# Performance work log

Measured on AMD Instinct MI355X. Metric: run time of the kernel, lower is better.

## Reference

```python
import math
import jax, jax.numpy as jnp
import numpy as np

N_HEADS = 16
TOPK_FACTOR = 0.5

def setup_inputs() -> dict:
    key = jax.random.key(0)
    ks = jax.random.split(key, 11)
    B, L, D = 2, 2048, 1024
    s = 0.02
    return {
        "q": jax.random.normal(ks[0], (B, L, D), jnp.float32),
        "k": jax.random.normal(ks[1], (B, L, D), jnp.float32),
        "v": jax.random.normal(ks[2], (B, L, D), jnp.float32),
        "Wq": jax.random.normal(ks[3], (D, D), jnp.float32) * s,
        "bq": jnp.zeros((D,), jnp.float32),
        "Wk": jax.random.normal(ks[4], (D, D), jnp.float32) * s,
        "bk": jnp.zeros((D,), jnp.float32),
        "Wv": jax.random.normal(ks[5], (D, D), jnp.float32) * s,
        "bv": jnp.zeros((D,), jnp.float32),
        "Wo": jax.random.normal(ks[6], (D, D), jnp.float32) * s,
        "bo": jnp.zeros((D,), jnp.float32),
    }

def reference(q, k, v, Wq, bq, Wk, bk, Wv, bv, Wo, bo):
    B, Lq, D = q.shape
    Lk = k.shape[1]
    H = N_HEADS
    d_k = D // H
    # projections -> [B, H, L, d_k]
    Q = (q @ Wq.T + bq).reshape(B, Lq, H, d_k).transpose(0, 2, 1, 3)
    K = (k @ Wk.T + bk).reshape(B, Lk, H, d_k).transpose(0, 2, 1, 3)
    V = (v @ Wv.T + bv).reshape(B, Lk, H, d_k).transpose(0, 2, 1, 3)
    # dense scores [B, H, Lq, Lk]
    scores = jnp.einsum("bhqd,bhkd->bhqk", Q, K) / math.sqrt(d_k)
    topk = max(1, int(TOPK_FACTOR * Lk))
    topk_scores, topk_idx = jax.lax.top_k(scores, topk)  # [B,H,Lq,topk]
    sm = jax.nn.softmax(topk_scores, axis=-1)
    # scatter softmax probs back into a zero [B,H,Lq,Lk] tensor (dropout in eval = identity)
    b_idx = jnp.arange(B)[:, None, None, None]
    h_idx = jnp.arange(H)[None, :, None, None]
    q_idx = jnp.arange(Lq)[None, None, :, None]
    attn = jnp.zeros_like(scores).at[b_idx, h_idx, q_idx, topk_idx].set(sm)
    ctx = jnp.einsum("bhqk,bhkd->bhqd", attn, V)
    ctx = ctx.transpose(0, 2, 1, 3).reshape(B, Lq, H * d_k)
    return ctx @ Wo.T + bo
```

## Files before the change

### kernel.cpp

```cpp
#include <hip/hip_runtime.h>
#include <math.h>

#define BATCH 2
#define SEQ 2048
#define DM 1024
#define NH 16
#define DH 64
#define TOPKN 1024
#define MROWS (BATCH * SEQ)

typedef float f32x4 __attribute__((ext_vector_type(4)));
typedef short s16x8 __attribute__((ext_vector_type(8)));
typedef short s16x4 __attribute__((ext_vector_type(4)));

#if __has_builtin(__builtin_amdgcn_mfma_f32_16x16x16_bf16)
#define MFMA1616(acc, a, b) acc = __builtin_amdgcn_mfma_f32_16x16x16_bf16(a, b, acc, 0, 0, 0)
#define MFMA1616_FENCE()
#elif __has_builtin(__builtin_amdgcn_mfma_f32_16x16x16bf16_1k)
#define MFMA1616(acc, a, b) acc = __builtin_amdgcn_mfma_f32_16x16x16bf16_1k(a, b, acc, 0, 0, 0)
#define MFMA1616_FENCE()
#else
#define MFMA1616(acc, a, b) \
  asm volatile("v_mfma_f32_16x16x16_bf16 %0, %1, %2, %0" : "+v"(acc) : "v"(a), "v"(b))
#define MFMA1616_FENCE() asm volatile("s_nop 7\ns_nop 7")
#endif

__device__ __forceinline__ unsigned short f2bf(float x) {
  unsigned u = __float_as_uint(x);
  return (unsigned short)((u + 0x7FFFu + ((u >> 16) & 1u)) >> 16);
}
__device__ __forceinline__ unsigned packHL(float x) {
  unsigned h = f2bf(x);
  float r = x - __uint_as_float(h << 16);
  unsigned l = f2bf(r);
  return h | (l << 16);
}

__global__ __launch_bounds__(256) void convW(const float* __restrict__ W,
                                             unsigned short* __restrict__ Whi,
                                             unsigned short* __restrict__ Wlo) {
  int i = (blockIdx.x * 256 + threadIdx.x) * 4;
  float4 x = *(const float4*)&W[i];
  float xs[4] = {x.x, x.y, x.z, x.w};
  union { s16x4 v; unsigned short s[4]; } hu, lu;
#pragma unroll
  for (int e = 0; e < 4; ++e) {
    unsigned short hb = f2bf(xs[e]);
    hu.s[e] = hb;
    lu.s[e] = f2bf(xs[e] - __uint_as_float((unsigned)hb << 16));
  }
  *(s16x4*)&Whi[i] = hu.v;
  *(s16x4*)&Wlo[i] = lu.v;
}

template <int ASRC, int MODE>
__global__ __launch_bounds__(256) void gemm_mfma(
    const void* __restrict__ Asrc, const unsigned short* __restrict__ Whi,
    const unsigned short* __restrict__ Wlo, const float* __restrict__ bias,
    void* __restrict__ out0, void* __restrict__ out1) {
  __shared__ unsigned short Ah[128][64], Al[128][64];
  __shared__ unsigned short Bh[64][64], Bl[64][64];

  const int f = blockIdx.x;
  const int xcd = f & 7, s = f >> 3;
  const int bm = xcd * 4 + (s >> 4);
  const int bn = s & 15;
  const int m0g = bm * 128, n0g = bn * 64;
  const int t = threadIdx.x, w = t >> 6, lane = t & 63;
  const int g = lane >> 4, c = lane & 15;
  const int wm = w >> 1, wn = w & 1;

  f32x4 acc[4][2];
#pragma unroll
  for (int i = 0; i < 4; ++i)
#pragma unroll
    for (int j = 0; j < 2; ++j) acc[i][j] = (f32x4){0.f, 0.f, 0.f, 0.f};

#pragma unroll 1
  for (int k0 = 0; k0 < 1024; k0 += 64) {
#pragma unroll
    for (int i = 0; i < 4; ++i) {
      int oid = t * 4 + i;
      int r = oid >> 3, j = oid & 7;
      union { s16x8 v; unsigned short sh[8]; } hu, lu;
      if (ASRC == 0) {
        const float* src = (const float*)Asrc + (size_t)(m0g + r) * 1024 + k0 + j * 8;
        float4 x0 = *(const float4*)src, x1 = *(const float4*)(src + 4);
        float xs[8] = {x0.x, x0.y, x0.z, x0.w, x1.x, x1.y, x1.z, x1.w};
#pragma unroll
        for (int e = 0; e < 8; ++e) {
          unsigned u = __float_as_uint(xs[e]);
          hu.sh[e] = (unsigned short)(u >> 16);
          lu.sh[e] = f2bf(xs[e] - __uint_as_float(u & 0xFFFF0000u));
        }
      } else {
        const unsigned* src = (const unsigned*)Asrc + (size_t)(m0g + r) * 1024 + k0 + j * 8;
        uint4 u0 = *(const uint4*)src, u1 = *(const uint4*)(src + 4);
        unsigned us[8] = {u0.x, u0.y, u0.z, u0.w, u1.x, u1.y, u1.z, u1.w};
#pragma unroll
        for (int e = 0; e < 8; ++e) {
          hu.sh[e] = (unsigned short)(us[e] & 0xFFFFu);
          lu.sh[e] = (unsigned short)(us[e] >> 16);
        }
      }
      int od = (j ^ (r & 7)) * 8;
      *(s16x8*)&Ah[r][od] = hu.v;
      *(s16x8*)&Al[r][od] = lu.v;
    }
#pragma unroll
    for (int i = 0; i < 4; ++i) {
      int oid = t * 4 + i;
      int pl = oid >> 9, idx = oid & 511, r = idx >> 3, j = idx & 7;
      const unsigned short* src = (pl ? Wlo : Whi) + (size_t)(n0g + r) * 1024 + k0 + j * 8;
      uint4 d = *(const uint4*)src;
      int od = (j ^ (r & 7)) * 8;
      if (pl) *(uint4*)&Bl[r][od] = d; else *(uint4*)&Bh[r][od] = d;
    }
    __syncthreads();
#pragma unroll
    for (int k2 = 0; k2 < 2; ++k2) {
      s16x8 ah[4], al4[4], bh[2], bl[2];
      int ob = ((k2 * 4 + g) ^ (c & 7)) * 8;
#pragma unroll
      for (int i = 0; i < 4; ++i) {
        int r = wm * 64 + i * 16 + c;
        ah[i] = *(const s16x8*)&Ah[r][ob];
        al4[i] = *(const s16x8*)&Al[r][ob];
      }
#pragma unroll
      for (int j = 0; j < 2; ++j) {
        int r = wn * 32 + j * 16 + c;
        bh[j] = *(const s16x8*)&Bh[r][ob];
        bl[j] = *(const s16x8*)&Bl[r][ob];
      }
#pragma unroll
      for (int i = 0; i < 4; ++i)
#pragma unroll
        for (int j = 0; j < 2; ++j) {
          acc[i][j] = __builtin_amdgcn_mfma_f32_16x16x32_bf16(ah[i], bh[j], acc[i][j], 0, 0, 0);
          acc[i][j] = __builtin_amdgcn_mfma_f32_16x16x32_bf16(ah[i], bl[j], acc[i][j], 0, 0, 0);
          acc[i][j] = __builtin_amdgcn_mfma_f32_16x16x32_bf16(al4[i], bh[j], acc[i][j], 0, 0, 0);
        }
    }
    __syncthreads();
  }

#pragma unroll
  for (int j = 0; j < 2; ++j) {
    const int col = n0g + wn * 32 + j * 16 + c;
    const float bj = bias[col];
#pragma unroll
    for (int i = 0; i < 4; ++i) {
      const int row0 = m0g + wm * 64 + i * 16 + g * 4;
      if (MODE == 0) {
        float* O = (float*)out0;
#pragma unroll
        for (int rr = 0; rr < 4; ++rr)
          O[(size_t)(row0 + rr) * 1024 + col] = acc[i][j][rr] + bj;
      } else if (MODE == 1) {
        unsigned* Q = (unsigned*)out0;
#pragma unroll
        for (int rr = 0; rr < 4; ++rr)
          Q[(size_t)(row0 + rr) * 1024 + col] = packHL((acc[i][j][rr] + bj) * 0.125f);
      } else if (MODE == 2) {
        unsigned short* Khi = (unsigned short*)out0;
        unsigned short* Klo = (unsigned short*)out1;
#pragma unroll
        for (int rr = 0; rr < 4; ++rr) {
          float x = acc[i][j][rr] + bj;
          unsigned short hb = f2bf(x);
          Khi[(size_t)(row0 + rr) * 1024 + col] = hb;
          Klo[(size_t)(row0 + rr) * 1024 + col] = f2bf(x - __uint_as_float((unsigned)hb << 16));
        }
      } else {
        unsigned short* Vt = (unsigned short*)out0;
        int b = row0 >> 11, l0 = row0 & (SEQ - 1);
        int h = col >> 6, dh = col & 63;
        union { s16x4 v; unsigned short sh[4]; } vv;
#pragma unroll
        for (int rr = 0; rr < 4; ++rr) vv.sh[rr] = f2bf(acc[i][j][rr] + bj);
        *(s16x4*)&Vt[(((size_t)b * NH + h) * DH + dh) * SEQ + l0] = vv.v;
      }
    }
  }
}

__global__ __launch_bounds__(512, 4) void attn_mfma(
    const unsigned* __restrict__ QHL, const unsigned short* __restrict__ Khi,
    const unsigned short* __restrict__ Klo, const unsigned short* __restrict__ Vt,
    unsigned* __restrict__ CtxP) {
  __shared__ __align__(16) char smem[16 * 1028 * 4];
  __shared__ __align__(16) unsigned Tlds[16];
  unsigned (*sc)[1028] = (unsigned(*)[1028])smem;
  float (*ctxp)[16][72] = (float(*)[16][72])smem;
  float (*szum)[8] = (float(*)[8])(smem + 8 * 16 * 72 * 4);

  int wg = blockIdx.x;
  wg = (wg & 7) * 512 + (wg >> 3);
  const int bh = wg >> 7, qt = wg & 127;
  const int b = bh >> 4, h = bh & 15;
  const int q0 = qt * 16;
  const int t = threadIdx.x, w = t >> 6, lane = t & 63;
  const int g = lane >> 4, c = lane & 15;
  const size_t rowb = (size_t)b * SEQ;

  s16x8 qhi[2], qlo[2];
  {
    const unsigned* qp = QHL + (rowb + q0 + c) * DM + h * DH + g * 8;
#pragma unroll
    for (int ds = 0; ds < 2; ++ds) {
      unsigned uw[8];
      *(uint4*)&uw[0] = *(const uint4*)(qp + ds * 32);
      *(uint4*)&uw[4] = *(const uint4*)(qp + ds * 32 + 4);
      union { s16x8 v; unsigned u[4]; } hi_, lo_;
#pragma unroll
      for (int p = 0; p < 4; ++p) {
        hi_.u[p] = (uw[2 * p] & 0xFFFFu) | (uw[2 * p + 1] << 16);
        lo_.u[p] = (uw[2 * p] >> 16) | (uw[2 * p + 1] & 0xFFFF0000u);
      }
      qhi[ds] = hi_.v; qlo[ds] = lo_.v;
    }
  }

  unsigned pk[16][2];
  {
    const f32x4 ZZ = (f32x4){0.f, 0.f, 0.f, 0.f};
    const size_t kcol = (size_t)h * DH + g * 8;
#pragma unroll
    for (int tt = 0; tt < 16; ++tt) {
      const size_t krow = (rowb + w * 256 + tt * 16 + c) * DM + kcol;
      s16x8 kh0 = *(const s16x8*)(Khi + krow);
      s16x8 kh1 = *(const s16x8*)(Khi + krow + 32);
      s16x8 kl0 = *(const s16x8*)(Klo + krow);
      s16x8 kl1 = *(const s16x8*)(Klo + krow + 32);
      f32x4 a = __builtin_amdgcn_mfma_f32_16x16x32_bf16(kh0, qhi[0], ZZ, 0, 0, 0);
      a = __builtin_amdgcn_mfma_f32_16x16x32_bf16(kh1, qhi[1], a, 0, 0, 0);
      a = __builtin_amdgcn_mfma_f32_16x16x32_bf16(kl0, qhi[0], a, 0, 0, 0);
      a = __builtin_amdgcn_mfma_f32_16x16x32_bf16(kl1, qhi[1], a, 0, 0, 0);
      a = __builtin_amdgcn_mfma_f32_16x16x32_bf16(kh0, qlo[0], a, 0, 0, 0);
      a = __builtin_amdgcn_mfma_f32_16x16x32_bf16(kh1, qlo[1], a, 0, 0, 0);
      unsigned u0 = (unsigned)fminf(fmaf(a[0], 8192.f, 32768.5f), 65535.f);
      unsigned u1 = (unsigned)fminf(fmaf(a[1], 8192.f, 32768.5f), 65535.f);
      unsigned u2 = (unsigned)fminf(fmaf(a[2], 8192.f, 32768.5f), 65535.f);
      unsigned u3 = (unsigned)fminf(fmaf(a[3], 8192.f, 32768.5f), 65535.f);
      pk[tt][0] = u0 | (u1 << 16);
      pk[tt][1] = u2 | (u3 << 16);
    }
  }

#pragma unroll
  for (int tt = 0; tt < 16; ++tt) {
    int col = w * 128 + tt * 8 + g * 2;
    sc[c][col] = pk[tt][0];
    sc[c][col + 1] = pk[tt][1];
  }
  __syncthreads();

  {
    const int r = 2 * w + (lane >> 5);
    const int hl = lane & 31;
    uint4 ts[8];
#pragma unroll
    for (int i = 0; i < 8; ++i)
      ts[i] = *(const uint4*)&sc[r][hl * 4 + i * 128];

    unsigned lo = 30720u, hi = 34816u;
#pragma unroll 1
    for (int it = 0; it < 12; ++it) {
      const unsigned mid = (lo + hi) >> 1;
      int cnt = 0;
#pragma unroll
      for (int i = 0; i < 8; ++i) {
        unsigned a0 = ts[i].x, a1 = ts[i].y, a2 = ts[i].z, a3 = ts[i].w;
        cnt += ((a0 & 0xFFFFu) >= mid) ? 1 : 0;
        cnt += ((a0 >> 16) >= mid) ? 1 : 0;
        cnt += ((a1 & 0xFFFFu) >= mid) ? 1 : 0;
        cnt += ((a1 >> 16) >= mid) ? 1 : 0;
        cnt += ((a2 & 0xFFFFu) >= mid) ? 1 : 0;
        cnt += ((a2 >> 16) >= mid) ? 1 : 0;
        cnt += ((a3 & 0xFFFFu) >= mid) ? 1 : 0;
        cnt += ((a3 >> 16) >= mid) ? 1 : 0;
      }
      cnt += __shfl_xor(cnt, 1);
      cnt += __shfl_xor(cnt, 2);
      cnt += __shfl_xor(cnt, 4);
      cnt += __shfl_xor(cnt, 8);
      cnt += __shfl_xor(cnt, 16);
      bool ge = cnt >= TOPKN;
      lo = ge ? mid : lo;
      hi = ge ? hi : mid;
    }
    if ((lane & 31) == 0) Tlds[r] = lo;
  }
  __syncthreads();
  const unsigned T = Tlds[c];

  const float C1 = 1.44269504f / 8192.0f;
  const float C2 = -49152.0f * (1.44269504f / 8192.0f);
  f32x4 opv[4];
#pragma unroll
  for (int j = 0; j < 4; ++j) opv[j] = (f32x4){0.f, 0.f, 0.f, 0.f};
  float z = 0.f;
  {
    const unsigned short* vb0 = Vt + ((size_t)bh * DH + c) * SEQ + w * 256 + g * 4;
#pragma unroll
    for (int kt = 0; kt < 16; ++kt) {
      unsigned p0 = pk[kt][0], p1 = pk[kt][1];
      unsigned u0 = p0 & 0xFFFFu, u1 = p0 >> 16;
      unsigned u2 = p1 & 0xFFFFu, u3 = p1 >> 16;
      float e0 = (u0 >= T) ? exp2f(fmaf((float)u0, C1, C2)) : 0.f;
      float e1 = (u1 >= T) ? exp2f(fmaf((float)u1, C1, C2)) : 0.f;
      float e2 = (u2 >= T) ? exp2f(fmaf((float)u2, C1, C2)) : 0.f;
      float e3 = (u3 >= T) ? exp2f(fmaf((float)u3, C1, C2)) : 0.f;
      z += (e0 + e1) + (e2 + e3);
      union { s16x4 v; unsigned u[2]; } pb;
      pb.u[0] = ((__float_as_uint(e0) + 0x8000u) >> 16) |
                ((__float_as_uint(e1) + 0x8000u) & 0xFFFF0000u);
      pb.u[1] = ((__float_as_uint(e2) + 0x8000u) >> 16) |
                ((__float_as_uint(e3) + 0x8000u) & 0xFFFF0000u);
#pragma unroll
      for (int j = 0; j < 4; ++j) {
        s16x4 va = *(const s16x4*)(vb0 + (size_t)j * 16 * SEQ + kt * 16);
        MFMA1616(opv[j], va, pb.v);
      }
    }
    MFMA1616_FENCE();
  }

  z += __shfl_xor(z, 16);
  z += __shfl_xor(z, 32);
  if (lane < 16) szum[c][w] = z;
#pragma unroll
  for (int j = 0; j < 4; ++j)
    *(f32x4*)&ctxp[w][c][j * 16 + g * 4] = opv[j];
  __syncthreads();
  if (w < 4) {
    float4 z0 = *(float4*)&szum[c][0];
    float4 z1 = *(float4*)&szum[c][4];
    float rinv = 1.f / (z0.x + z0.y + z0.z + z0.w + z1.x + z1.y + z1.z + z1.w);
    f32x4 ssum = (f32x4){0.f, 0.f, 0.f, 0.f};
#pragma unroll
    for (int w2 = 0; w2 < 8; ++w2)
      ssum += *(const f32x4*)&ctxp[w2][c][w * 16 + g * 4];
    unsigned ov[4];
    ov[0] = packHL(ssum[0] * rinv);
    ov[1] = packHL(ssum[1] * rinv);
    ov[2] = packHL(ssum[2] * rinv);
    ov[3] = packHL(ssum[3] * rinv);
    *(uint4*)&CtxP[(rowb + q0 + c) * DM + h * DH + w * 16 + g * 4] = *(uint4*)&ov[0];
  }
}

extern "C" void kernel_launch(void* const* d_in, const int* in_sizes, int n_in,
                              void* d_out, int out_size, void* d_ws, size_t ws_size,
                              hipStream_t stream) {
  const float* q  = (const float*)d_in[0];
  const float* k  = (const float*)d_in[1];
  const float* v  = (const float*)d_in[2];
  const float* Wq = (const float*)d_in[3];
  const float* bq = (const float*)d_in[4];
  const float* Wk = (const float*)d_in[5];
  const float* bk = (const float*)d_in[6];
  const float* Wv = (const float*)d_in[7];
  const float* bv = (const float*)d_in[8];
  const float* Wo = (const float*)d_in[9];
  const float* bo = (const float*)d_in[10];
  float* out = (float*)d_out;

  char* ws = (char*)d_ws;
  unsigned* QHL       = (unsigned*)ws;
  unsigned short* Khi = (unsigned short*)(ws + (16u << 20));
  unsigned short* Klo = (unsigned short*)(ws + (24u << 20));
  unsigned short* Vt  = (unsigned short*)(ws + (32u << 20));
  unsigned short* Whi = (unsigned short*)(ws + (40u << 20));
  unsigned short* Wlo = (unsigned short*)(ws + (42u << 20));

  convW<<<1024, 256, 0, stream>>>(Wq, Whi, Wlo);
  gemm_mfma<0, 1><<<512, 256, 0, stream>>>(q, Whi, Wlo, bq, QHL, nullptr);
  convW<<<1024, 256, 0, stream>>>(Wk, Whi, Wlo);
  gemm_mfma<0, 2><<<512, 256, 0, stream>>>(k, Whi, Wlo, bk, Khi, Klo);
  convW<<<1024, 256, 0, stream>>>(Wv, Whi, Wlo);
  gemm_mfma<0, 3><<<512, 256, 0, stream>>>(v, Whi, Wlo, bv, Vt, nullptr);
  attn_mfma<<<BATCH * NH * (SEQ / 16), 512, 0, stream>>>(QHL, Khi, Klo, Vt, QHL);
  convW<<<1024, 256, 0, stream>>>(Wo, Whi, Wlo);
  gemm_mfma<1, 0><<<512, 256, 0, stream>>>(QHL, Whi, Wlo, bo, out, nullptr);
}
```

Before: 710.2 us.

## Process 32 query rows per attention block to reuse K/V tiles

The attention kernel now handles 32 queries per workgroup with 1024 threads (16 waves), each wave covering 128 keys for two 16-row query tiles. Each K and V fragment loaded from global memory feeds two query tiles, halving K/V global traffic per query. The cost is a larger workgroup, more registers per thread (double accumulators and packed scores), and a reduction across 16 partial contexts in shared memory. Fewer, larger blocks may reduce occupancy and latency hiding.

```diff
diff --git a/kernel.cpp b/kernel.cpp
--- a/kernel.cpp
+++ b/kernel.cpp
@@ -185,28 +185,29 @@
   }
 }
 
-__global__ __launch_bounds__(512, 4) void attn_mfma(
+__global__ __launch_bounds__(1024, 4) void attn_mfma(
     const unsigned* __restrict__ QHL, const unsigned short* __restrict__ Khi,
     const unsigned short* __restrict__ Klo, const unsigned short* __restrict__ Vt,
     unsigned* __restrict__ CtxP) {
-  __shared__ __align__(16) char smem[16 * 1028 * 4];
-  __shared__ __align__(16) unsigned Tlds[16];
+  __shared__ __align__(16) char smem[16 * 32 * 66 * 4];
+  __shared__ __align__(16) float szum[32][16];
+  __shared__ unsigned Tlds[32];
   unsigned (*sc)[1028] = (unsigned(*)[1028])smem;
-  float (*ctxp)[16][72] = (float(*)[16][72])smem;
-  float (*szum)[8] = (float(*)[8])(smem + 8 * 16 * 72 * 4);
+  float (*ctxp)[32][66] = (float(*)[32][66])smem;
 
   int wg = blockIdx.x;
-  wg = (wg & 7) * 512 + (wg >> 3);
-  const int bh = wg >> 7, qt = wg & 127;
+  wg = (wg & 7) * 256 + (wg >> 3);
+  const int bh = wg >> 6, qt = wg & 63;
   const int b = bh >> 4, h = bh & 15;
-  const int q0 = qt * 16;
-  const int t = threadIdx.x, w = t >> 6, lane = t & 63;
+  const int q0 = qt * 32;
+  const int t = threadIdx.x, wid = t >> 6, lane = t & 63;
   const int g = lane >> 4, c = lane & 15;
   const size_t rowb = (size_t)b * SEQ;
 
-  s16x8 qhi[2], qlo[2];
-  {
-    const unsigned* qp = QHL + (rowb + q0 + c) * DM + h * DH + g * 8;
+  s16x8 qhiA[2], qloA[2], qhiB[2], qloB[2];
+#pragma unroll
+  for (int qh = 0; qh < 2; ++qh) {
+    const unsigned* qp = QHL + (rowb + q0 + qh * 16 + c) * DM + h * DH + g * 8;
 #pragma unroll
     for (int ds = 0; ds < 2; ++ds) {
       unsigned uw[8];
@@ -218,46 +219,59 @@
         hi_.u[p] = (uw[2 * p] & 0xFFFFu) | (uw[2 * p + 1] << 16);
         lo_.u[p] = (uw[2 * p] >> 16) | (uw[2 * p + 1] & 0xFFFF0000u);
       }
-      qhi[ds] = hi_.v; qlo[ds] = lo_.v;
-    }
-  }
-
-  unsigned pk[16][2];
+      if (qh == 0) { qhiA[ds] = hi_.v; qloA[ds] = lo_.v; }
+      else         { qhiB[ds] = hi_.v; qloB[ds] = lo_.v; }
+    }
+  }
+
+  unsigned pkA[8][2], pkB[8][2];
   {
     const f32x4 ZZ = (f32x4){0.f, 0.f, 0.f, 0.f};
     const size_t kcol = (size_t)h * DH + g * 8;
 #pragma unroll
-    for (int tt = 0; tt < 16; ++tt) {
-      const size_t krow = (rowb + w * 256 + tt * 16 + c) * DM + kcol;
+    for (int tt = 0; tt < 8; ++tt) {
+      const size_t krow = (rowb + wid * 128 + tt * 16 + c) * DM + kcol;
       s16x8 kh0 = *(const s16x8*)(Khi + krow);
       s16x8 kh1 = *(const s16x8*)(Khi + krow + 32);
       s16x8 kl0 = *(const s16x8*)(Klo + krow);
       s16x8 kl1 = *(const s16x8*)(Klo + krow + 32);
-      f32x4 a = __builtin_amdgcn_mfma_f32_16x16x32_bf16(kh0, qhi[0], ZZ, 0, 0, 0);
-      a = __builtin_amdgcn_mfma_f32_16x16x32_bf16(kh1, qhi[1], a, 0, 0, 0);
-      a = __builtin_amdgcn_mfma_f32_16x16x32_bf16(kl0, qhi[0], a, 0, 0, 0);
-      a = __builtin_amdgcn_mfma_f32_16x16x32_bf16(kl1, qhi[1], a, 0, 0, 0);
-      a = __builtin_amdgcn_mfma_f32_16x16x32_bf16(kh0, qlo[0], a, 0, 0, 0);
-      a = __builtin_amdgcn_mfma_f32_16x16x32_bf16(kh1, qlo[1], a, 0, 0, 0);
-      unsigned u0 = (unsigned)fminf(fmaf(a[0], 8192.f, 32768.5f), 65535.f);
-      unsigned u1 = (unsigned)fminf(fmaf(a[1], 8192.f, 32768.5f), 65535.f);
-      unsigned u2 = (unsigned)fminf(fmaf(a[2], 8192.f, 32768.5f), 65535.f);
-      unsigned u3 = (unsigned)fminf(fmaf(a[3], 8192.f, 32768.5f), 65535.f);
-      pk[tt][0] = u0 | (u1 << 16);
-      pk[tt][1] = u2 | (u3 << 16);
-    }
-  }
-
-#pragma unroll
-  for (int tt = 0; tt < 16; ++tt) {
-    int col = w * 128 + tt * 8 + g * 2;
-    sc[c][col] = pk[tt][0];
-    sc[c][col + 1] = pk[tt][1];
+      f32x4 aA = __builtin_amdgcn_mfma_f32_16x16x32_bf16(kh0, qhiA[0], ZZ, 0, 0, 0);
+      f32x4 aB = __builtin_amdgcn_mfma_f32_16x16x32_bf16(kh0, qhiB[0], ZZ, 0, 0, 0);
+      aA = __builtin_amdgcn_mfma_f32_16x16x32_bf16(kh1, qhiA[1], aA, 0, 0, 0);
+      aB = __builtin_amdgcn_mfma_f32_16x16x32_bf16(kh1, qhiB[1], aB, 0, 0, 0);
+      aA = __builtin_amdgcn_mfma_f32_16x16x32_bf16(kl0, qhiA[0], aA, 0, 0, 0);
+      aB = __builtin_amdgcn_mfma_f32_16x16x32_bf16(kl0, qhiB[0], aB, 0, 0, 0);
+      aA = __builtin_amdgcn_mfma_f32_16x16x32_bf16(kl1, qhiA[1], aA, 0, 0, 0);
+      aB = __builtin_amdgcn_mfma_f32_16x16x32_bf16(kl1, qhiB[1], aB, 0, 0, 0);
+      aA = __builtin_amdgcn_mfma_f32_16x16x32_bf16(kh0, qloA[0], aA, 0, 0, 0);
+      aB = __builtin_amdgcn_mfma_f32_16x16x32_bf16(kh0, qloB[0], aB, 0, 0, 0);
+      aA = __builtin_amdgcn_mfma_f32_16x16x32_bf16(kh1, qloA[1], aA, 0, 0, 0);
+      aB = __builtin_amdgcn_mfma_f32_16x16x32_bf16(kh1, qloB[1], aB, 0, 0, 0);
+      unsigned a0 = (unsigned)fminf(fmaf(aA[0], 8192.f, 32768.5f), 65535.f);
+      unsigned a1 = (unsigned)fminf(fmaf(aA[1], 8192.f, 32768.5f), 65535.f);
+      unsigned a2 = (unsigned)fminf(fmaf(aA[2], 8192.f, 32768.5f), 65535.f);
+      unsigned a3 = (unsigned)fminf(fmaf(aA[3], 8192.f, 32768.5f), 65535.f);
+      pkA[tt][0] = a0 | (a1 << 16);
+      pkA[tt][1] = a2 | (a3 << 16);
+      unsigned b0 = (unsigned)fminf(fmaf(aB[0], 8192.f, 32768.5f), 65535.f);
+      unsigned b1 = (unsigned)fminf(fmaf(aB[1], 8192.f, 32768.5f), 65535.f);
+      unsigned b2 = (unsigned)fminf(fmaf(aB[2], 8192.f, 32768.5f), 65535.f);
+      unsigned b3 = (unsigned)fminf(fmaf(aB[3], 8192.f, 32768.5f), 65535.f);
+      pkB[tt][0] = b0 | (b1 << 16);
+      pkB[tt][1] = b2 | (b3 << 16);
+    }
+  }
+
+#pragma unroll
+  for (int tt = 0; tt < 8; ++tt) {
+    int col = wid * 64 + tt * 8 + g * 2;
+    *(uint2*)&sc[c][col] = make_uint2(pkA[tt][0], pkA[tt][1]);
+    *(uint2*)&sc[c + 16][col] = make_uint2(pkB[tt][0], pkB[tt][1]);
   }
   __syncthreads();
 
   {
-    const int r = 2 * w + (lane >> 5);
+    const int r = 2 * wid + (lane >> 5);
     const int hl = lane & 31;
     uint4 ts[8];
 #pragma unroll
@@ -293,61 +307,92 @@
     if ((lane & 31) == 0) Tlds[r] = lo;
   }
   __syncthreads();
-  const unsigned T = Tlds[c];
+  const unsigned TA = Tlds[c];
+  const unsigned TB = Tlds[c + 16];
 
   const float C1 = 1.44269504f / 8192.0f;
   const float C2 = -49152.0f * (1.44269504f / 8192.0f);
-  f32x4 opv[4];
-#pragma unroll
-  for (int j = 0; j < 4; ++j) opv[j] = (f32x4){0.f, 0.f, 0.f, 0.f};
-  float z = 0.f;
+  f32x4 opvA[4], opvB[4];
+#pragma unroll
+  for (int j = 0; j < 4; ++j) {
+    opvA[j] = (f32x4){0.f, 0.f, 0.f, 0.f};
+    opvB[j] = (f32x4){0.f, 0.f, 0.f, 0.f};
+  }
+  float zA = 0.f, zB = 0.f;
   {
-    const unsigned short* vb0 = Vt + ((size_t)bh * DH + c) * SEQ + w * 256 + g * 4;
-#pragma unroll
-    for (int kt = 0; kt < 16; ++kt) {
-      unsigned p0 = pk[kt][0], p1 = pk[kt][1];
-      unsigned u0 = p0 & 0xFFFFu, u1 = p0 >> 16;
-      unsigned u2 = p1 & 0xFFFFu, u3 = p1 >> 16;
-      float e0 = (u0 >= T) ? exp2f(fmaf((float)u0, C1, C2)) : 0.f;
-      float e1 = (u1 >= T) ? exp2f(fmaf((float)u1, C1, C2)) : 0.f;
-      float e2 = (u2 >= T) ? exp2f(fmaf((float)u2, C1, C2)) : 0.f;
-      float e3 = (u3 >= T) ? exp2f(fmaf((float)u3, C1, C2)) : 0.f;
-      z += (e0 + e1) + (e2 + e3);
-      union { s16x4 v; unsigned u[2]; } pb;
-      pb.u[0] = ((__float_as_uint(e0) + 0x8000u) >> 16) |
-                ((__float_as_uint(e1) + 0x8000u) & 0xFFFF0000u);
-      pb.u[1] = ((__float_as_uint(e2) + 0x8000u) >> 16) |
-                ((__float_as_uint(e3) + 0x8000u) & 0xFFFF0000u);
+    const unsigned short* vb0 = Vt + ((size_t)bh * DH + c) * SEQ + wid * 128 + g * 4;
+#pragma unroll
+    for (int kt = 0; kt < 8; ++kt) {
+      unsigned pa0 = pkA[kt][0], pa1 = pkA[kt][1];
+      unsigned ua0 = pa0 & 0xFFFFu, ua1 = pa0 >> 16;
+      unsigned ua2 = pa1 & 0xFFFFu, ua3 = pa1 >> 16;
+      float ea0 = (ua0 >= TA) ? exp2f(fmaf((float)ua0, C1, C2)) : 0.f;
+      float ea1 = (ua1 >= TA) ? exp2f(fmaf((float)ua1, C1, C2)) : 0.f;
+      float ea2 = (ua2 >= TA) ? exp2f(fmaf((float)ua2, C1, C2)) : 0.f;
+      float ea3 = (ua3 >= TA) ? exp2f(fmaf((float)ua3, C1, C2)) : 0.f;
+      zA += (ea0 + ea1) + (ea2 + ea3);
+      union { s16x4 v; unsigned u[2]; } pbA;
+      pbA.u[0] = ((__float_as_uint(ea0) + 0x8000u) >> 16) |
+                 ((__float_as_uint(ea1) + 0x8000u) & 0xFFFF0000u);
+      pbA.u[1] = ((__float_as_uint(ea2) + 0x8000u) >> 16) |
+                 ((__float_as_uint(ea3) + 0x8000u) & 0xFFFF0000u);
+      unsigned pb0 = pkB[kt][0], pb1 = pkB[kt][1];
+      unsigned ub0 = pb0 & 0xFFFFu, ub1 = pb0 >> 16;
+      unsigned ub2 = pb1 & 0xFFFFu, ub3 = pb1 >> 16;
+      float eb0 = (ub0 >= TB) ? exp2f(fmaf((float)ub0, C1, C2)) : 0.f;
+      float eb1 = (ub1 >= TB) ? exp2f(fmaf((float)ub1, C1, C2)) : 0.f;
+      float eb2 = (ub2 >= TB) ? exp2f(fmaf((float)ub2, C1, C2)) : 0.f;
+      float eb3 = (ub3 >= TB) ? exp2f(fmaf((float)ub3, C1, C2)) : 0.f;
+      zB += (eb0 + eb1) + (eb2 + eb3);
+      union { s16x4 v; unsigned u[2]; } pbB;
+      pbB.u[0] = ((__float_as_uint(eb0) + 0x8000u) >> 16) |
+                 ((__float_as_uint(eb1) + 0x8000u) & 0xFFFF0000u);
+      pbB.u[1] = ((__float_as_uint(eb2) + 0x8000u) >> 16) |
+                 ((__float_as_uint(eb3) + 0x8000u) & 0xFFFF0000u);
 #pragma unroll
       for (int j = 0; j < 4; ++j) {
         s16x4 va = *(const s16x4*)(vb0 + (size_t)j * 16 * SEQ + kt * 16);
-        MFMA1616(opv[j], va, pb.v);
+        MFMA1616(opvA[j], va, pbA.v);
+        MFMA1616(opvB[j], va, pbB.v);
       }
     }
     MFMA1616_FENCE();
   }
 
-  z += __shfl_xor(z, 16);
-  z += __shfl_xor(z, 32);
-  if (lane < 16) szum[c][w] = z;
-#pragma unroll
-  for (int j = 0; j < 4; ++j)
-    *(f32x4*)&ctxp[w][c][j * 16 + g * 4] = opv[j];
+  zA += __shfl_xor(zA, 16);
+  zA += __shfl_xor(zA, 32);
+  zB += __shfl_xor(zB, 16);
+  zB += __shfl_xor(zB, 32);
+  if (lane < 16) {
+    szum[c][wid] = zA;
+    szum[c + 16][wid] = zB;
+  }
   __syncthreads();
-  if (w < 4) {
-    float4 z0 = *(float4*)&szum[c][0];
-    float4 z1 = *(float4*)&szum[c][4];
-    float rinv = 1.f / (z0.x + z0.y + z0.z + z0.w + z1.x + z1.y + z1.z + z1.w);
+#pragma unroll
+  for (int j = 0; j < 4; ++j) {
+    *(f32x4*)&ctxp[wid][c][j * 16 + g * 4] = opvA[j];
+    *(f32x4*)&ctxp[wid][c + 16][j * 16 + g * 4] = opvB[j];
+  }
+  __syncthreads();
+
+  if (t < 512) {
+    const int q = t >> 4, d4 = t & 15;
+    float4 z0 = *(float4*)&szum[q][0];
+    float4 z1 = *(float4*)&szum[q][4];
+    float4 z2 = *(float4*)&szum[q][8];
+    float4 z3 = *(float4*)&szum[q][12];
+    float rinv = 1.f / ((z0.x + z0.y + z0.z + z0.w) + (z1.x + z1.y + z1.z + z1.w) +
+                        (z2.x + z2.y + z2.z + z2.w) + (z3.x + z3.y + z3.z + z3.w));
     f32x4 ssum = (f32x4){0.f, 0.f, 0.f, 0.f};
 #pragma unroll
-    for (int w2 = 0; w2 < 8; ++w2)
-      ssum += *(const f32x4*)&ctxp[w2][c][w * 16 + g * 4];
+    for (int w2 = 0; w2 < 16; ++w2)
+      ssum += *(const f32x4*)&ctxp[w2][q][d4 * 4];
     unsigned ov[4];
     ov[0] = packHL(ssum[0] * rinv);
     ov[1] = packHL(ssum[1] * rinv);
     ov[2] = packHL(ssum[2] * rinv);
     ov[3] = packHL(ssum[3] * rinv);
-    *(uint4*)&CtxP[(rowb + q0 + c) * DM + h * DH + w * 16 + g * 4] = *(uint4*)&ov[0];
+    *(uint4*)&CtxP[(rowb + q0 + q) * DM + h * DH + d4 * 4] = *(uint4*)&ov[0];
   }
 }
 
@@ -381,7 +426,7 @@
   gemm_mfma<0, 2><<<512, 256, 0, stream>>>(k, Whi, Wlo, bk, Khi, Klo);
   convW<<<1024, 256, 0, stream>>>(Wv, Whi, Wlo);
   gemm_mfma<0, 3><<<512, 256, 0, stream>>>(v, Whi, Wlo, bv, Vt, nullptr);
-  attn_mfma<<<BATCH * NH * (SEQ / 16), 512, 0, stream>>>(QHL, Khi, Klo, Vt, QHL);
+  attn_mfma<<<BATCH * NH * (SEQ / 32), 1024, 0, stream>>>(QHL, Khi, Klo, Vt, QHL);
   convW<<<1024, 256, 0, stream>>>(Wo, Whi, Wlo);
   gemm_mfma<1, 0><<<512, 256, 0, stream>>>(QHL, Whi, Wlo, bo, out, nullptr);
 }
```

Measured after the change: 653.1 us (median of 2 runs). 1.09x faster.
